# Performance work log

Hardware: AMD Instinct MI355X
Metric: run time of the kernel (lower is better)

## Reference

```python
import jax, jax.numpy as jnp
import numpy as np

B, T, D_MODEL, D_HIDDEN = 4, 8192, 1024, 1024
EPS = 1e-5

def setup_inputs() -> dict:
    key = jax.random.key(0)
    ks = jax.random.split(key, 8)
    s_in = 1.0 / np.sqrt(D_MODEL)
    s_h = 1.0 / np.sqrt(D_HIDDEN)
    return {
        "x": jax.random.normal(ks[0], (B, T, D_MODEL), jnp.float32),
        "W_ih": jax.random.uniform(ks[1], (D_MODEL, D_HIDDEN), jnp.float32, -s_in, s_in),
        "b_ih": jnp.zeros((D_HIDDEN,), jnp.float32),
        "W_gate": jax.random.uniform(ks[2], (D_MODEL, D_HIDDEN), jnp.float32, -s_in, s_in),
        "b_gate": jnp.zeros((D_HIDDEN,), jnp.float32),
        "log_a": jnp.full((D_HIDDEN,), -0.1, jnp.float32),
        "ln_g": jnp.ones((D_HIDDEN,), jnp.float32),
        "ln_b": jnp.zeros((D_HIDDEN,), jnp.float32),
        "W_out": jax.random.uniform(ks[3], (D_HIDDEN, D_HIDDEN), jnp.float32, -s_h, s_h),
        "b_out": jnp.zeros((D_HIDDEN,), jnp.float32),
        "W_proj": jax.random.uniform(ks[4], (D_HIDDEN, D_MODEL), jnp.float32, -s_h, s_h),
        "b_proj": jnp.zeros((D_MODEL,), jnp.float32),
    }

def _scan(alpha, beta):
    # h_t = alpha_t * h_{t-1} + beta_t, h_0 = 0, over axis 1 (time)
    def combine(c1, c2):
        a1, b1 = c1
        a2, b2 = c2
        return a2 * a1, a2 * b1 + b2
    _, h = jax.lax.associative_scan(combine, (alpha, beta), axis=1)
    return h

def reference(x, W_ih, b_ih, W_gate, b_gate, log_a, ln_g, ln_b, W_out, b_out, W_proj, b_proj):
    ih = jnp.einsum("btd,dh->bth", x, W_ih) + b_ih
    gate = jax.nn.sigmoid(jnp.einsum("btd,dh->bth", x, W_gate) + b_gate)
    a = jnp.exp(log_a)  # [H]
    alpha = (1.0 - gate) * a  # [B,T,H]
    beta = gate * ih
    h = _scan(alpha, beta)
    # LayerNorm over last dim
    mu = jnp.mean(h, axis=-1, keepdims=True)
    var = jnp.var(h, axis=-1, keepdims=True)
    hn = (h - mu) * jax.lax.rsqrt(var + EPS) * ln_g + ln_b
    out = jnp.einsum("bth,ho->bto", hn, W_out) + b_out
    return jnp.einsum("bth,hd->btd", out, W_proj) + b_proj
```

## Files before the change

kernel.cpp:

```cpp
#include <hip/hip_runtime.h>

typedef short bhalf8 __attribute__((ext_vector_type(8)));
typedef float floatx4 __attribute__((ext_vector_type(4)));
typedef unsigned short ushortx8 __attribute__((ext_vector_type(8)));

__device__ __forceinline__ unsigned short f2bf(float f){
  union { float f; unsigned int u; } v; v.f = f;
  unsigned int u = v.u;
  u += 0x7fffu + ((u >> 16) & 1u);
  return (unsigned short)(u >> 16);
}
__device__ __forceinline__ float bf2f(unsigned short u){
  union { unsigned int u; float f; } v; v.u = ((unsigned)u) << 16; return v.f;
}
__device__ __forceinline__ unsigned pack2(float a, float b){
  return (unsigned)f2bf(a) | ((unsigned)f2bf(b) << 16);
}

__device__ __forceinline__ void async16(const unsigned short* g, unsigned short* l){
  __builtin_amdgcn_global_load_lds(
      (const __attribute__((address_space(1))) void*)g,
      (__attribute__((address_space(3))) void*)l,
      16, 0, 0);
}

template<int EPI>
__global__ __launch_bounds__(256) void gemm_k(
    const unsigned short* __restrict__ Ab, const unsigned short* __restrict__ BT,
    const float* __restrict__ bias, float* __restrict__ Cf,
    unsigned short* __restrict__ Cb, int K, int ldc)
{
  __shared__ __align__(16) unsigned short As[128*64];
  __shared__ __align__(16) unsigned short Bs[128*64];
  const int tid = threadIdx.x;
  const int n0 = blockIdx.x * 128;
  const int m0 = blockIdx.y * 128;
  const int wid = tid >> 6, lane = tid & 63;
  const int wr = (wid >> 1) * 64, wc = (wid & 1) * 64;
  const int r16 = lane & 15, quad = lane >> 4;
  const int ldsbase = (tid & ~63) * 8;

  const unsigned short* pA[4];
  const unsigned short* pB[4];
  #pragma unroll
  for (int i = 0; i < 4; ++i) {
    int p = tid + i*256;
    int row = p >> 3;
    int cp = (p & 7) ^ (row & 7);
    pA[i] = Ab + (size_t)(m0+row)*K + cp*8;
    pB[i] = BT + (size_t)(n0+row)*K + cp*8;
  }
  int aoff[2][4], boff[2][4];
  #pragma unroll
  for (int ks = 0; ks < 2; ++ks){
    #pragma unroll
    for (int mi = 0; mi < 4; ++mi){
      int row = wr + mi*16 + r16;
      aoff[ks][mi] = (row*8 + ((ks*4+quad) ^ (row&7))) * 8;
    }
    #pragma unroll
    for (int ni = 0; ni < 4; ++ni){
      int row = wc + ni*16 + r16;
      boff[ks][ni] = (row*8 + ((ks*4+quad) ^ (row&7))) * 8;
    }
  }

  floatx4 acc[4][4];
  #pragma unroll
  for (int i=0;i<4;i++)
    #pragma unroll
    for (int j=0;j<4;j++) acc[i][j] = {0.f,0.f,0.f,0.f};

  for (int k0 = 0; k0 < K; k0 += 64) {
    #pragma unroll
    for (int i = 0; i < 4; ++i) async16(pA[i], &As[ldsbase + i*2048]);
    #pragma unroll
    for (int i = 0; i < 4; ++i) async16(pB[i], &Bs[ldsbase + i*2048]);
    __syncthreads();
    #pragma unroll
    for (int ks = 0; ks < 2; ++ks) {
      bhalf8 aF[4], bF[4];
      #pragma unroll
      for (int mi=0;mi<4;++mi) aF[mi] = *(const bhalf8*)&As[aoff[ks][mi]];
      #pragma unroll
      for (int ni=0;ni<4;++ni) bF[ni] = *(const bhalf8*)&Bs[boff[ks][ni]];
      #pragma unroll
      for (int mi=0;mi<4;++mi)
        #pragma unroll
        for (int ni=0;ni<4;++ni)
          acc[mi][ni] = __builtin_amdgcn_mfma_f32_16x16x32_bf16(aF[mi], bF[ni], acc[mi][ni], 0, 0, 0);
    }
    __syncthreads();
    #pragma unroll
    for (int i = 0; i < 4; ++i) { pA[i] += 64; pB[i] += 64; }
  }

  #pragma unroll
  for (int mi=0;mi<4;++mi)
    #pragma unroll
    for (int ni=0;ni<4;++ni)
      #pragma unroll
      for (int r=0;r<4;++r){
        int m = m0 + wr + mi*16 + quad*4 + r;
        int n = n0 + wc + ni*16 + r16;
        float val = acc[mi][ni][r];
        if (EPI == 0) Cf[(size_t)m*ldc + n] = val;
        else if (EPI == 1) Cf[(size_t)m*ldc + n] = val + bias[n];
        else if (EPI == 3) Cb[(size_t)m*ldc + n] = f2bf(val + bias[n]);
        else Cb[(size_t)n*ldc + m] = f2bf(val);
      }
}

__global__ __launch_bounds__(256) void transpose_cvt(const float* __restrict__ src,
                                                     unsigned short* __restrict__ dst,
                                                     int R, int C)
{
  __shared__ float tile[32][33];
  int c0 = blockIdx.x*32, r0 = blockIdx.y*32;
  int tx = threadIdx.x, ty = threadIdx.y;
  #pragma unroll
  for (int i=0;i<32;i+=8)
    tile[ty+i][tx] = src[(size_t)(r0+ty+i)*C + c0+tx];
  __syncthreads();
  #pragma unroll
  for (int i=0;i<32;i+=8)
    dst[(size_t)(c0+ty+i)*R + r0+tx] = f2bf(tile[tx][ty+i]);
}

__global__ __launch_bounds__(256) void cvt_f32_bf16(const float* __restrict__ src,
                                                    unsigned short* __restrict__ dst)
{
  int idx = (blockIdx.x*256 + threadIdx.x) * 4;
  float4 v = *(const float4*)(src + idx);
  uint2 p;
  p.x = pack2(v.x, v.y);
  p.y = pack2(v.z, v.w);
  *(uint2*)(dst + idx) = p;
}

__global__ __launch_bounds__(256) void prep_small(const float* __restrict__ b_out,
                                                  const float* __restrict__ W_proj,
                                                  const float* __restrict__ b_proj,
                                                  const float* __restrict__ log_a,
                                                  const float* __restrict__ b_ih,
                                                  const float* __restrict__ b_gate,
                                                  float* __restrict__ b_comb,
                                                  float* __restrict__ a_vec,
                                                  float* __restrict__ bcat)
{
  int d = blockIdx.x*256 + threadIdx.x;
  if (d < 1024) {
    float acc = b_proj[d];
    for (int e = 0; e < 1024; ++e)
      acc += b_out[e] * W_proj[(size_t)e*1024 + d];
    b_comb[d] = acc;
    a_vec[d] = __expf(log_a[d]);
    bcat[d] = b_ih[d];
  } else {
    bcat[d] = b_gate[d-1024];
  }
}

__device__ __forceinline__ void ab_step(unsigned short iu, unsigned short gu,
                                        float a, float& al, float& be)
{
  float zi = bf2f(iu), zg = bf2f(gu);
  float g = 1.f / (1.f + __expf(-zg));
  al = (1.f - g) * a;
  be = g * zi;
}

__global__ __launch_bounds__(256, 4) void scan_phase1(const unsigned short* __restrict__ pre,
    const float* __restrict__ a_vec, float* __restrict__ Asum, float* __restrict__ Ssum)
{
  int wid = threadIdx.x >> 6, lane = threadIdx.x & 63;
  int u = blockIdx.x*4 + wid;
  int b = u >> 10, c = u & 1023;
  int ch0 = lane*16;
  float a[16], A[16], S[16];
  #pragma unroll
  for (int q=0;q<4;++q) *(float4*)&a[q*4] = *(const float4*)(a_vec + ch0 + q*4);
  #pragma unroll
  for (int j=0;j<16;++j){ A[j]=1.f; S[j]=0.f; }
  size_t base = ((size_t)(b*8192 + c*8))*2048 + ch0;
  for (int t=0;t<8;++t){
    ushortx8 i0 = *(const ushortx8*)(pre + base);
    ushortx8 i1 = *(const ushortx8*)(pre + base + 8);
    ushortx8 g0 = *(const ushortx8*)(pre + base + 1024);
    ushortx8 g1 = *(const ushortx8*)(pre + base + 1032);
    #pragma unroll
    for (int j=0;j<8;++j){
      float al, be;
      ab_step(i0[j], g0[j], a[j], al, be);
      A[j] *= al; S[j] = al*S[j] + be;
      ab_step(i1[j], g1[j], a[j+8], al, be);
      A[j+8] *= al; S[j+8] = al*S[j+8] + be;
    }
    base += 2048;
  }
  size_t o = (size_t)u*1024 + ch0;
  #pragma unroll
  for (int q=0;q<4;++q){
    *(float4*)(Asum + o + q*4) = *(const float4*)&A[q*4];
    *(float4*)(Ssum + o + q*4) = *(const float4*)&S[q*4];
  }
}

__global__ __launch_bounds__(256) void scan_phase2(const float* __restrict__ Asum,
    const float* __restrict__ Ssum, float* __restrict__ carry)
{
  int idx = blockIdx.x*256 + threadIdx.x;
  int b = idx >> 10, n = idx & 1023;
  float cur = 0.f;
  size_t o = (size_t)b*1024*1024 + n;
  for (int c = 0; c < 1024; ++c) {
    carry[o] = cur;
    cur = Asum[o]*cur + Ssum[o];
    o += 1024;
  }
}

__global__ __launch_bounds__(256, 4) void scan_phase3(const unsigned short* __restrict__ pre,
    const float* __restrict__ a_vec, const float* __restrict__ carry,
    const float* __restrict__ ln_g, const float* __restrict__ ln_b,
    unsigned short* __restrict__ hn)
{
  int wid = threadIdx.x >> 6, lane = threadIdx.x & 63;
  int u = blockIdx.x*4 + wid;
  int b = u >> 10, c = u & 1023;
  int ch0 = lane*16;
  float a[16], h[16], g[16], lb[16];
  #pragma unroll
  for (int q=0;q<4;++q){
    *(float4*)&a[q*4]  = *(const float4*)(a_vec + ch0 + q*4);
    *(float4*)&h[q*4]  = *(const float4*)(carry + (size_t)u*1024 + ch0 + q*4);
    *(float4*)&g[q*4]  = *(const float4*)(ln_g + ch0 + q*4);
    *(float4*)&lb[q*4] = *(const float4*)(ln_b + ch0 + q*4);
  }
  size_t base  = ((size_t)(b*8192 + c*8))*2048 + ch0;
  size_t hbase = ((size_t)(b*8192 + c*8))*1024 + ch0;
  for (int t=0;t<8;++t){
    ushortx8 i0 = *(const ushortx8*)(pre + base);
    ushortx8 i1 = *(const ushortx8*)(pre + base + 8);
    ushortx8 g0 = *(const ushortx8*)(pre + base + 1024);
    ushortx8 g1 = *(const ushortx8*)(pre + base + 1032);
    float s = 0.f, s2 = 0.f;
    #pragma unroll
    for (int j=0;j<8;++j){
      float al, be;
      ab_step(i0[j], g0[j], a[j], al, be);
      h[j] = al*h[j] + be;
      s += h[j]; s2 += h[j]*h[j];
      ab_step(i1[j], g1[j], a[j+8], al, be);
      h[j+8] = al*h[j+8] + be;
      s += h[j+8]; s2 += h[j+8]*h[j+8];
    }
    #pragma unroll
    for (int off = 32; off > 0; off >>= 1) {
      s  += __shfl_xor(s,  off);
      s2 += __shfl_xor(s2, off);
    }
    float mu = s * (1.f/1024.f);
    float var = s2 * (1.f/1024.f) - mu*mu;
    float rstd = rsqrtf(var + 1e-5f);
    uint4 o0, o1;
    float v0, v1;
    v0 = (h[0]-mu)*rstd*g[0]+lb[0];  v1 = (h[1]-mu)*rstd*g[1]+lb[1];  o0.x = pack2(v0,v1);
    v0 = (h[2]-mu)*rstd*g[2]+lb[2];  v1 = (h[3]-mu)*rstd*g[3]+lb[3];  o0.y = pack2(v0,v1);
    v0 = (h[4]-mu)*rstd*g[4]+lb[4];  v1 = (h[5]-mu)*rstd*g[5]+lb[5];  o0.z = pack2(v0,v1);
    v0 = (h[6]-mu)*rstd*g[6]+lb[6];  v1 = (h[7]-mu)*rstd*g[7]+lb[7];  o0.w = pack2(v0,v1);
    v0 = (h[8]-mu)*rstd*g[8]+lb[8];  v1 = (h[9]-mu)*rstd*g[9]+lb[9];  o1.x = pack2(v0,v1);
    v0 = (h[10]-mu)*rstd*g[10]+lb[10]; v1 = (h[11]-mu)*rstd*g[11]+lb[11]; o1.y = pack2(v0,v1);
    v0 = (h[12]-mu)*rstd*g[12]+lb[12]; v1 = (h[13]-mu)*rstd*g[13]+lb[13]; o1.z = pack2(v0,v1);
    v0 = (h[14]-mu)*rstd*g[14]+lb[14]; v1 = (h[15]-mu)*rstd*g[15]+lb[15]; o1.w = pack2(v0,v1);
    *(uint4*)(hn + hbase)     = o0;
    *(uint4*)(hn + hbase + 8) = o1;
    base += 2048; hbase += 1024;
  }
}

extern "C" void kernel_launch(void* const* d_in, const int* in_sizes, int n_in,
                              void* d_out, int out_size, void* d_ws, size_t ws_size,
                              hipStream_t stream)
{
  const float* x      = (const float*)d_in[0];
  const float* W_ih   = (const float*)d_in[1];
  const float* b_ih   = (const float*)d_in[2];
  const float* W_gate = (const float*)d_in[3];
  const float* b_gate = (const float*)d_in[4];
  const float* log_a  = (const float*)d_in[5];
  const float* ln_g   = (const float*)d_in[6];
  const float* ln_b   = (const float*)d_in[7];
  const float* W_out  = (const float*)d_in[8];
  const float* b_out  = (const float*)d_in[9];
  const float* W_proj = (const float*)d_in[10];
  const float* b_proj = (const float*)d_in[11];
  float* out = (float*)d_out;

  char* ws = (char*)d_ws;
  size_t off = 0;
  auto alloc = [&](size_t bytes)->char* {
    char* p = ws + off; off += (bytes + 255) & ~(size_t)255; return p;
  };
  unsigned short* pre   = (unsigned short*)alloc((size_t)32768*2048*2);
  unsigned short* hn    = (unsigned short*)alloc((size_t)32768*1024*2);
  unsigned short* xb    = hn;
  unsigned short* WcatT = (unsigned short*)alloc((size_t)2048*1024*2);
  unsigned short* WprojT= (unsigned short*)alloc((size_t)1024*1024*2);
  unsigned short* Woutb = (unsigned short*)alloc((size_t)1024*1024*2);
  unsigned short* WcombT= (unsigned short*)alloc((size_t)1024*1024*2);
  float* Asum           = (float*)alloc((size_t)4*1024*1024*4);
  float* Ssum           = (float*)alloc((size_t)4*1024*1024*4);
  float* carry          = (float*)alloc((size_t)4*1024*1024*4);
  float* b_comb         = (float*)alloc(1024*4);
  float* a_vec          = (float*)alloc(1024*4);
  float* bcat           = (float*)alloc(2048*4);

  dim3 t32x8(32, 8);
  transpose_cvt<<<dim3(32,32), t32x8, 0, stream>>>(W_ih,   WcatT,              1024, 1024);
  transpose_cvt<<<dim3(32,32), t32x8, 0, stream>>>(W_gate, WcatT + 1024*1024,  1024, 1024);
  transpose_cvt<<<dim3(32,32), t32x8, 0, stream>>>(W_proj, WprojT,             1024, 1024);
  cvt_f32_bf16<<<1024, 256, 0, stream>>>(W_out, Woutb);
  prep_small<<<8, 256, 0, stream>>>(b_out, W_proj, b_proj, log_a, b_ih, b_gate,
                                    b_comb, a_vec, bcat);
  cvt_f32_bf16<<<32768, 256, 0, stream>>>(x, xb);
  gemm_k<2><<<dim3(8,8), 256, 0, stream>>>(Woutb, WprojT, nullptr, nullptr, WcombT, 1024, 1024);
  gemm_k<3><<<dim3(16,256), 256, 0, stream>>>(xb, WcatT, bcat, nullptr, pre, 1024, 2048);
  scan_phase1<<<1024, 256, 0, stream>>>(pre, a_vec, Asum, Ssum);
  scan_phase2<<<16, 256, 0, stream>>>(Asum, Ssum, carry);
  scan_phase3<<<1024, 256, 0, stream>>>(pre, a_vec, carry, ln_g, ln_b, hn);
  gemm_k<1><<<dim3(8,256), 256, 0, stream>>>(hn, WcombT, b_comb, out, nullptr, 1024, 1024);
}
```

Measured before the change: 752.1 us.

## Remap GEMM blocks per XCD, fuse prep kernels, lengthen scan chunks

```diff
diff --git a/kernel.cpp b/kernel.cpp
--- a/kernel.cpp
+++ b/kernel.cpp
@@ -33,8 +33,16 @@
   __shared__ __align__(16) unsigned short As[128*64];
   __shared__ __align__(16) unsigned short Bs[128*64];
   const int tid = threadIdx.x;
-  const int n0 = blockIdx.x * 128;
-  const int m0 = blockIdx.y * 128;
+
+  const int nbx = gridDim.x;
+  const int nwg = nbx * gridDim.y;
+  const int flat = blockIdx.y * nbx + blockIdx.x;
+  const int xcd = flat & 7, j = flat >> 3;
+  const int q = nwg >> 3, r = nwg & 7;
+  const int logical = (xcd < r ? xcd * (q + 1) : r * (q + 1) + (xcd - r) * q) + j;
+  const int n0 = (logical % nbx) * 128;
+  const int m0 = (logical / nbx) * 128;
+
   const int wid = tid >> 6, lane = tid & 63;
   const int wr = (wid >> 1) * 64, wc = (wid & 1) * 64;
   const int r16 = lane & 15, quad = lane >> 4;
@@ -69,7 +77,7 @@
   #pragma unroll
   for (int i=0;i<4;i++)
     #pragma unroll
-    for (int j=0;j<4;j++) acc[i][j] = {0.f,0.f,0.f,0.f};
+    for (int j2=0;j2<4;j2++) acc[i][j2] = {0.f,0.f,0.f,0.f};
 
   for (int k0 = 0; k0 < K; k0 += 64) {
     #pragma unroll
@@ -100,10 +108,10 @@
     #pragma unroll
     for (int ni=0;ni<4;++ni)
       #pragma unroll
-      for (int r=0;r<4;++r){
-        int m = m0 + wr + mi*16 + quad*4 + r;
+      for (int rr=0;rr<4;++rr){
+        int m = m0 + wr + mi*16 + quad*4 + rr;
         int n = n0 + wc + ni*16 + r16;
-        float val = acc[mi][ni][r];
+        float val = acc[mi][ni][rr];
         if (EPI == 0) Cf[(size_t)m*ldc + n] = val;
         else if (EPI == 1) Cf[(size_t)m*ldc + n] = val + bias[n];
         else if (EPI == 3) Cb[(size_t)m*ldc + n] = f2bf(val + bias[n]);
@@ -111,20 +119,53 @@
       }
 }
 
-__global__ __launch_bounds__(256) void transpose_cvt(const float* __restrict__ src,
-                                                     unsigned short* __restrict__ dst,
-                                                     int R, int C)
+__global__ __launch_bounds__(256) void prep_all(
+    const float* __restrict__ W_ih, const float* __restrict__ W_gate,
+    const float* __restrict__ W_proj, const float* __restrict__ W_out,
+    const float* __restrict__ b_out, const float* __restrict__ b_proj,
+    const float* __restrict__ log_a, const float* __restrict__ b_ih,
+    const float* __restrict__ b_gate,
+    unsigned short* __restrict__ WcatT, unsigned short* __restrict__ WprojT,
+    unsigned short* __restrict__ Woutb,
+    float* __restrict__ b_comb, float* __restrict__ a_vec, float* __restrict__ bcat)
 {
   __shared__ float tile[32][33];
-  int c0 = blockIdx.x*32, r0 = blockIdx.y*32;
-  int tx = threadIdx.x, ty = threadIdx.y;
-  #pragma unroll
-  for (int i=0;i<32;i+=8)
-    tile[ty+i][tx] = src[(size_t)(r0+ty+i)*C + c0+tx];
-  __syncthreads();
-  #pragma unroll
-  for (int i=0;i<32;i+=8)
-    dst[(size_t)(c0+ty+i)*R + r0+tx] = f2bf(tile[tx][ty+i]);
+  const int blk = blockIdx.x;
+  const int tid = threadIdx.x;
+  if (blk < 3072) {
+    const int which = blk >> 10;
+    const int t = blk & 1023;
+    const float* src = (which == 0) ? W_ih : (which == 1) ? W_gate : W_proj;
+    unsigned short* dst = (which == 0) ? WcatT : (which == 1) ? (WcatT + 1024*1024) : WprojT;
+    const int c0 = (t & 31) * 32, r0 = (t >> 5) * 32;
+    const int tx = tid & 31, ty = tid >> 5;
+    #pragma unroll
+    for (int i = 0; i < 32; i += 8)
+      tile[ty+i][tx] = src[(size_t)(r0+ty+i)*1024 + c0+tx];
+    __syncthreads();
+    #pragma unroll
+    for (int i = 0; i < 32; i += 8)
+      dst[(size_t)(c0+ty+i)*1024 + r0+tx] = f2bf(tile[tx][ty+i]);
+  } else if (blk < 4096) {
+    int idx = ((blk - 3072)*256 + tid) * 4;
+    float4 v = *(const float4*)(W_out + idx);
+    uint2 p;
+    p.x = pack2(v.x, v.y);
+    p.y = pack2(v.z, v.w);
+    *(uint2*)(Woutb + idx) = p;
+  } else {
+    int d = (blk - 4096)*256 + tid;
+    if (d < 1024) {
+      float acc = b_proj[d];
+      for (int e = 0; e < 1024; ++e)
+        acc += b_out[e] * W_proj[(size_t)e*1024 + d];
+      b_comb[d] = acc;
+      a_vec[d] = __expf(log_a[d]);
+      bcat[d] = b_ih[d];
+    } else {
+      bcat[d] = b_gate[d-1024];
+    }
+  }
 }
 
 __global__ __launch_bounds__(256) void cvt_f32_bf16(const float* __restrict__ src,
@@ -138,28 +179,8 @@
   *(uint2*)(dst + idx) = p;
 }
 
-__global__ __launch_bounds__(256) void prep_small(const float* __restrict__ b_out,
-                                                  const float* __restrict__ W_proj,
-                                                  const float* __restrict__ b_proj,
-                                                  const float* __restrict__ log_a,
-                                                  const float* __restrict__ b_ih,
-                                                  const float* __restrict__ b_gate,
-                                                  float* __restrict__ b_comb,
-                                                  float* __restrict__ a_vec,
-                                                  float* __restrict__ bcat)
-{
-  int d = blockIdx.x*256 + threadIdx.x;
-  if (d < 1024) {
-    float acc = b_proj[d];
-    for (int e = 0; e < 1024; ++e)
-      acc += b_out[e] * W_proj[(size_t)e*1024 + d];
-    b_comb[d] = acc;
-    a_vec[d] = __expf(log_a[d]);
-    bcat[d] = b_ih[d];
-  } else {
-    bcat[d] = b_gate[d-1024];
-  }
-}
+#define CHUNK 32
+#define NCHUNK 256
 
 __device__ __forceinline__ void ab_step(unsigned short iu, unsigned short gu,
                                         float a, float& al, float& be)
@@ -175,15 +196,15 @@
 {
   int wid = threadIdx.x >> 6, lane = threadIdx.x & 63;
   int u = blockIdx.x*4 + wid;
-  int b = u >> 10, c = u & 1023;
+  int b = u >> 8, c = u & (NCHUNK-1);
   int ch0 = lane*16;
   float a[16], A[16], S[16];
   #pragma unroll
   for (int q=0;q<4;++q) *(float4*)&a[q*4] = *(const float4*)(a_vec + ch0 + q*4);
   #pragma unroll
   for (int j=0;j<16;++j){ A[j]=1.f; S[j]=0.f; }
-  size_t base = ((size_t)(b*8192 + c*8))*2048 + ch0;
-  for (int t=0;t<8;++t){
+  size_t base = ((size_t)(b*8192 + c*CHUNK))*2048 + ch0;
+  for (int t=0;t<CHUNK;++t){
     ushortx8 i0 = *(const ushortx8*)(pre + base);
     ushortx8 i1 = *(const ushortx8*)(pre + base + 8);
     ushortx8 g0 = *(const ushortx8*)(pre + base + 1024);
@@ -212,8 +233,8 @@
   int idx = blockIdx.x*256 + threadIdx.x;
   int b = idx >> 10, n = idx & 1023;
   float cur = 0.f;
-  size_t o = (size_t)b*1024*1024 + n;
-  for (int c = 0; c < 1024; ++c) {
+  size_t o = (size_t)b*NCHUNK*1024 + n;
+  for (int c = 0; c < NCHUNK; ++c) {
     carry[o] = cur;
     cur = Asum[o]*cur + Ssum[o];
     o += 1024;
@@ -227,7 +248,7 @@
 {
   int wid = threadIdx.x >> 6, lane = threadIdx.x & 63;
   int u = blockIdx.x*4 + wid;
-  int b = u >> 10, c = u & 1023;
+  int b = u >> 8, c = u & (NCHUNK-1);
   int ch0 = lane*16;
   float a[16], h[16], g[16], lb[16];
   #pragma unroll
@@ -237,9 +258,9 @@
     *(float4*)&g[q*4]  = *(const float4*)(ln_g + ch0 + q*4);
     *(float4*)&lb[q*4] = *(const float4*)(ln_b + ch0 + q*4);
   }
-  size_t base  = ((size_t)(b*8192 + c*8))*2048 + ch0;
-  size_t hbase = ((size_t)(b*8192 + c*8))*1024 + ch0;
-  for (int t=0;t<8;++t){
+  size_t base  = ((size_t)(b*8192 + c*CHUNK))*2048 + ch0;
+  size_t hbase = ((size_t)(b*8192 + c*CHUNK))*1024 + ch0;
+  for (int t=0;t<CHUNK;++t){
     ushortx8 i0 = *(const ushortx8*)(pre + base);
     ushortx8 i1 = *(const ushortx8*)(pre + base + 8);
     ushortx8 g0 = *(const ushortx8*)(pre + base + 1024);
@@ -309,25 +330,21 @@
   unsigned short* WprojT= (unsigned short*)alloc((size_t)1024*1024*2);
   unsigned short* Woutb = (unsigned short*)alloc((size_t)1024*1024*2);
   unsigned short* WcombT= (unsigned short*)alloc((size_t)1024*1024*2);
-  float* Asum           = (float*)alloc((size_t)4*1024*1024*4);
-  float* Ssum           = (float*)alloc((size_t)4*1024*1024*4);
-  float* carry          = (float*)alloc((size_t)4*1024*1024*4);
+  float* Asum           = (float*)alloc((size_t)1024*1024*4);
+  float* Ssum           = (float*)alloc((size_t)1024*1024*4);
+  float* carry          = (float*)alloc((size_t)1024*1024*4);
   float* b_comb         = (float*)alloc(1024*4);
   float* a_vec          = (float*)alloc(1024*4);
   float* bcat           = (float*)alloc(2048*4);
 
-  dim3 t32x8(32, 8);
-  transpose_cvt<<<dim3(32,32), t32x8, 0, stream>>>(W_ih,   WcatT,              1024, 1024);
-  transpose_cvt<<<dim3(32,32), t32x8, 0, stream>>>(W_gate, WcatT + 1024*1024,  1024, 1024);
-  transpose_cvt<<<dim3(32,32), t32x8, 0, stream>>>(W_proj, WprojT,             1024, 1024);
-  cvt_f32_bf16<<<1024, 256, 0, stream>>>(W_out, Woutb);
-  prep_small<<<8, 256, 0, stream>>>(b_out, W_proj, b_proj, log_a, b_ih, b_gate,
-                                    b_comb, a_vec, bcat);
+  prep_all<<<4104, 256, 0, stream>>>(W_ih, W_gate, W_proj, W_out, b_out, b_proj,
+                                     log_a, b_ih, b_gate,
+                                     WcatT, WprojT, Woutb, b_comb, a_vec, bcat);
   cvt_f32_bf16<<<32768, 256, 0, stream>>>(x, xb);
   gemm_k<2><<<dim3(8,8), 256, 0, stream>>>(Woutb, WprojT, nullptr, nullptr, WcombT, 1024, 1024);
   gemm_k<3><<<dim3(16,256), 256, 0, stream>>>(xb, WcatT, bcat, nullptr, pre, 1024, 2048);
-  scan_phase1<<<1024, 256, 0, stream>>>(pre, a_vec, Asum, Ssum);
+  scan_phase1<<<256, 256, 0, stream>>>(pre, a_vec, Asum, Ssum);
   scan_phase2<<<16, 256, 0, stream>>>(Asum, Ssum, carry);
-  scan_phase3<<<1024, 256, 0, stream>>>(pre, a_vec, carry, ln_g, ln_b, hn);
+  scan_phase3<<<256, 256, 0, stream>>>(pre, a_vec, carry, ln_g, ln_b, hn);
   gemm_k<1><<<dim3(8,256), 256, 0, stream>>>(hn, WcombT, b_comb, out, nullptr, 1024, 1024);
 }
```

Result: faster. 690.3 us (-8.2%).
